# Kernel optimization log

Measured on AMD Instinct MI355X. Metric: run time of the kernel, lower is better.

The kernel has to match this reference:

```python
import jax, jax.numpy as jnp
import numpy as np

N = 50000      # nodes
E = 800000     # edges
G = 512        # graphs in batch
F0 = 92        # orig atom feature len
F = 64         # atom_fea_len
NB = 41        # nbr_fea_len
H = 128        # h_fea_len
NCONV = 3
EPS = 1e-5


def setup_inputs() -> dict:
    key = jax.random.key(0)
    ks = jax.random.split(key, 16)
    s = 0.05
    inp = {
        "x": jax.random.normal(ks[0], (N, F0), jnp.float32),
        "edge_index": jax.random.randint(ks[1], (2, E), 0, N),
        "edge_attr": jax.random.normal(ks[2], (E, NB), jnp.float32),
        "batch": jnp.sort(jax.random.randint(ks[3], (N,), 0, G)),
        # embedding (only applied at the first conv, when x width == F0)
        "emb_W": jax.random.normal(ks[4], (F0, F), jnp.float32) * s,
        "emb_b": jnp.zeros((F,), jnp.float32),
        # per-conv-layer params, stacked on leading axis
        "bn1_g": jnp.ones((NCONV, F), jnp.float32),
        "bn1_b": jnp.zeros((NCONV, F), jnp.float32),
        "bn2_g": jnp.ones((NCONV, F), jnp.float32),
        "bn2_b": jnp.zeros((NCONV, F), jnp.float32),
        "lnf_W": jax.random.normal(ks[5], (NCONV, 2 * F + NB, F), jnp.float32) * s,
        "lnf_b": jnp.zeros((NCONV, F), jnp.float32),
        "lns_W": jax.random.normal(ks[6], (NCONV, 2 * F + NB, F), jnp.float32) * s,
        "lns_b": jnp.zeros((NCONV, F), jnp.float32),
        # readout MLP
        "fc1_W": jax.random.normal(ks[7], (F, H), jnp.float32) * s,
        "fc1_b": jnp.zeros((H,), jnp.float32),
        "out_W": jax.random.normal(ks[8], (H, 1), jnp.float32) * s,
        "out_b": jnp.zeros((1,), jnp.float32),
    }
    return inp


def _batchnorm(x, g, b):
    # training-mode BatchNorm1d: batch stats over node dim, biased variance
    mean = jnp.mean(x, axis=0)
    var = jnp.var(x, axis=0)
    return (x - mean) * jax.lax.rsqrt(var + EPS) * g + b


def _cgconv(x, edge_index, edge_attr, bn1_g, bn1_b, bn2_g, bn2_b, Wf, bf, Ws, bs):
    x = _batchnorm(x, bn1_g, bn1_b)
    # flow='target_to_source': x_i = x[edge_index[0]], x_j = x[edge_index[1]],
    # aggregation scatter-adds messages to edge_index[0]
    src, dst = edge_index[0], edge_index[1]
    z = jnp.concatenate([x[src], x[dst], edge_attr], axis=-1)   # [E, 2F+NB]
    m = jax.nn.sigmoid(z @ Wf + bf) * jax.nn.softplus(z @ Ws + bs)
    agg = jax.ops.segment_sum(m, src, num_segments=x.shape[0])  # [N, F]
    out = _batchnorm(agg, bn2_g, bn2_b) + x
    return jax.nn.softplus(out)


def reference(x, edge_index, edge_attr, batch, emb_W, emb_b,
              bn1_g, bn1_b, bn2_g, bn2_b, lnf_W, lnf_b, lns_W, lns_b,
              fc1_W, fc1_b, out_W, out_b):
    h = x @ emb_W + emb_b  # first conv applies embedding (x width == F0)
    for i in range(NCONV):
        h = _cgconv(h, edge_index, edge_attr,
                    bn1_g[i], bn1_b[i], bn2_g[i], bn2_b[i],
                    lnf_W[i], lnf_b[i], lns_W[i], lns_b[i])
    # global mean pool per graph
    sums = jax.ops.segment_sum(h, batch, num_segments=G)
    cnts = jax.ops.segment_sum(jnp.ones((h.shape[0], 1), h.dtype), batch, num_segments=G)
    crys = sums / jnp.maximum(cnts, 1.0)                         # [G, F]
    crys = jax.nn.softplus(jax.nn.softplus(crys) @ fc1_W + fc1_b)
    return crys @ out_W + out_b                                  # [G, 1]
```

## Files before the change

kernel.cpp:

```cpp
#include <hip/hip_runtime.h>

#define NN 50000
#define NE 800000
#define NG 512
#define F0 92
#define FF 64
#define NB 41
#define HH 128

__device__ __forceinline__ float softplusf(float x) {
    return fmaxf(x, 0.f) + __logf(1.f + __expf(-fabsf(x)));
}
__device__ __forceinline__ float sigmoidf(float x) {
    return __fdividef(1.f, 1.f + __expf(-x));
}

__global__ __launch_bounds__(256) void emb_kernel(
    const float* __restrict__ x, const float* __restrict__ W,
    const float* __restrict__ bias, float* __restrict__ h)
{
    __shared__ float sx[4][F0];
    const int lane = threadIdx.x & 63;
    const int w = threadIdx.x >> 6;
    float wr[F0];
#pragma unroll
    for (int k = 0; k < F0; ++k) wr[k] = W[k * FF + lane];
    const float bv = bias[lane];
    const int nit = NN / 4;
    for (int it = blockIdx.x; it < nit; it += gridDim.x) {
        const int n = it * 4 + w;
        if (lane < 46) {
            sx[w][lane * 2]     = x[n * F0 + lane * 2];
            sx[w][lane * 2 + 1] = x[n * F0 + lane * 2 + 1];
        }
        __syncthreads();
        float acc = bv;
#pragma unroll
        for (int k4 = 0; k4 < F0 / 4; ++k4) {
            float4 q = *(const float4*)&sx[w][k4 * 4];
            acc = fmaf(q.x, wr[k4 * 4 + 0], acc);
            acc = fmaf(q.y, wr[k4 * 4 + 1], acc);
            acc = fmaf(q.z, wr[k4 * 4 + 2], acc);
            acc = fmaf(q.w, wr[k4 * 4 + 3], acc);
        }
        h[n * FF + lane] = acc;
        __syncthreads();
    }
}

__global__ __launch_bounds__(256) void stats_kernel(
    const float* __restrict__ src, float* __restrict__ stats)
{
    __shared__ float sd[2][4][FF];
    const int f = threadIdx.x & 63;
    const int r = threadIdx.x >> 6;
    float s = 0.f, s2 = 0.f;
    for (int n = blockIdx.x * 4 + r; n < NN; n += gridDim.x * 4) {
        float v = src[n * FF + f];
        s += v;
        s2 = fmaf(v, v, s2);
    }
    sd[0][r][f] = s;
    sd[1][r][f] = s2;
    __syncthreads();
    if (threadIdx.x < FF) {
        float ts = sd[0][0][f] + sd[0][1][f] + sd[0][2][f] + sd[0][3][f];
        float t2 = sd[1][0][f] + sd[1][1][f] + sd[1][2][f] + sd[1][3][f];
        atomicAdd(&stats[f], ts);
        atomicAdd(&stats[FF + f], t2);
    }
}

__global__ void finalize_kernel(const float* __restrict__ g, const float* __restrict__ b,
                                float* __restrict__ stats)
{
    const int f = threadIdx.x;
    const float inv = 1.f / (float)NN;
    float mean = stats[f] * inv;
    float var = stats[FF + f] * inv - mean * mean;
    float rstd = rsqrtf(var + 1e-5f);
    float A = rstd * g[f];
    stats[2 * FF + f] = A;
    stats[3 * FF + f] = fmaf(-mean, A, b[f]);
}

__global__ __launch_bounds__(256) void node_kernel(
    const float* __restrict__ h, const float* __restrict__ stats,
    const float* __restrict__ Wf, const float* __restrict__ Ws,
    float* __restrict__ xn,
    float* __restrict__ pSf, float* __restrict__ pDf,
    float* __restrict__ pSs, float* __restrict__ pDs)
{
    __shared__ float sx[4][FF];
    const int lane = threadIdx.x & 63;
    const int w = threadIdx.x >> 6;
    const float* W = (w < 2) ? Wf : Ws;
    const int rowbase = (w & 1) * FF;
    float wr[FF];
#pragma unroll
    for (int k = 0; k < FF; ++k) wr[k] = W[(rowbase + k) * FF + lane];
    const float A = stats[2 * FF + lane];
    const float B = stats[3 * FF + lane];
    float* outp = (w == 0) ? pSf : (w == 1) ? pDf : (w == 2) ? pSs : pDs;
    for (int n = blockIdx.x; n < NN; n += gridDim.x) {
        const float xv = fmaf(h[n * FF + lane], A, B);
        if (w == 0) xn[n * FF + lane] = xv;
        sx[w][lane] = xv;
        __syncthreads();
        float acc = 0.f;
#pragma unroll
        for (int k4 = 0; k4 < FF / 4; ++k4) {
            float4 q = *(const float4*)&sx[w][k4 * 4];
            acc = fmaf(q.x, wr[k4 * 4 + 0], acc);
            acc = fmaf(q.y, wr[k4 * 4 + 1], acc);
            acc = fmaf(q.z, wr[k4 * 4 + 2], acc);
            acc = fmaf(q.w, wr[k4 * 4 + 3], acc);
        }
        outp[n * FF + lane] = acc;
        __syncthreads();
    }
}

__global__ __launch_bounds__(256) void edge_kernel(
    const int* __restrict__ ei, const float* __restrict__ ea,
    const float* __restrict__ Wf, const float* __restrict__ Ws,
    const float* __restrict__ bf, const float* __restrict__ bs,
    const float* __restrict__ pSf, const float* __restrict__ pDf,
    const float* __restrict__ pSs, const float* __restrict__ pDs,
    float* __restrict__ agg)
{
    __shared__ float sea[4][44];
    const int lane = threadIdx.x & 63;
    const int w = threadIdx.x >> 6;
    float wfr[44], wsr[44];
#pragma unroll
    for (int k = 0; k < 44; ++k) {
        wfr[k] = (k < NB) ? Wf[(2 * FF + k) * FF + lane] : 0.f;
        wsr[k] = (k < NB) ? Ws[(2 * FF + k) * FF + lane] : 0.f;
    }
    const float bfv = bf[lane], bsv = bs[lane];
    const int nit = NE / 4;
    for (int it = blockIdx.x; it < nit; it += gridDim.x) {
        const int e = it * 4 + w;
        const int src = ei[e];
        const int dst = ei[NE + e];
        const float gSf = pSf[src * FF + lane];
        const float gDf = pDf[dst * FF + lane];
        const float gSs = pSs[src * FF + lane];
        const float gDs = pDs[dst * FF + lane];
        float v = 0.f;
        if (lane < NB) v = ea[(size_t)e * NB + lane];
        if (lane < 44) sea[w][lane] = v;
        __syncthreads();
        float accF = bfv, accS = bsv;
#pragma unroll
        for (int k4 = 0; k4 < 11; ++k4) {
            float4 q = *(const float4*)&sea[w][k4 * 4];
            accF = fmaf(q.x, wfr[k4 * 4 + 0], accF); accS = fmaf(q.x, wsr[k4 * 4 + 0], accS);
            accF = fmaf(q.y, wfr[k4 * 4 + 1], accF); accS = fmaf(q.y, wsr[k4 * 4 + 1], accS);
            accF = fmaf(q.z, wfr[k4 * 4 + 2], accF); accS = fmaf(q.z, wsr[k4 * 4 + 2], accS);
            accF = fmaf(q.w, wfr[k4 * 4 + 3], accF); accS = fmaf(q.w, wsr[k4 * 4 + 3], accS);
        }
        const float m = sigmoidf(accF + gSf + gDf) * softplusf(accS + gSs + gDs);
        unsafeAtomicAdd(&agg[src * FF + lane], m);
    }
}

__global__ __launch_bounds__(256) void update_kernel(
    const float* __restrict__ agg, const float* __restrict__ xn,
    const float* __restrict__ stats, float* __restrict__ h,
    const int* __restrict__ batch, float* __restrict__ pool,
    float* __restrict__ pcnt, const int do_pool)
{
    const int total = NN * FF;
    for (int idx = blockIdx.x * blockDim.x + threadIdx.x; idx < total;
         idx += gridDim.x * blockDim.x) {
        const int f = idx & 63;
        const int n = idx >> 6;
        const float A = stats[2 * FF + f];
        const float B = stats[3 * FF + f];
        const float v = softplusf(fmaf(agg[idx], A, B) + xn[idx]);
        if (do_pool) {
            const int g = batch[n];
            unsafeAtomicAdd(&pool[g * FF + f], v);
            if (f == 0) unsafeAtomicAdd(&pcnt[g], 1.f);
        } else {
            h[idx] = v;
        }
    }
}

__global__ __launch_bounds__(128) void readout_kernel(
    const float* __restrict__ pool, const float* __restrict__ pcnt,
    const float* __restrict__ fc1W, const float* __restrict__ fc1b,
    const float* __restrict__ outW, const float* __restrict__ outb,
    float* __restrict__ out)
{
    __shared__ float sp[FF];
    __shared__ float red[2];
    const int g = blockIdx.x;
    const int t = threadIdx.x;
    if (t < FF) {
        const float c = fmaxf(pcnt[g], 1.f);
        sp[t] = softplusf(pool[g * FF + t] / c);
    }
    __syncthreads();
    float a = fc1b[t];
#pragma unroll
    for (int k = 0; k < FF; ++k) a = fmaf(sp[k], fc1W[k * HH + t], a);
    float o = softplusf(a) * outW[t];
#pragma unroll
    for (int off = 32; off > 0; off >>= 1) o += __shfl_down(o, off, 64);
    if ((t & 63) == 0) red[t >> 6] = o;
    __syncthreads();
    if (t == 0) out[g] = red[0] + red[1] + outb[0];
}

extern "C" void kernel_launch(void* const* d_in, const int* in_sizes, int n_in,
                              void* d_out, int out_size, void* d_ws, size_t ws_size,
                              hipStream_t stream)
{
    const float* x     = (const float*)d_in[0];
    const int*   ei    = (const int*)  d_in[1];
    const float* ea    = (const float*)d_in[2];
    const int*   batch = (const int*)  d_in[3];
    const float* embW  = (const float*)d_in[4];
    const float* embb  = (const float*)d_in[5];
    const float* bn1g  = (const float*)d_in[6];
    const float* bn1b  = (const float*)d_in[7];
    const float* bn2g  = (const float*)d_in[8];
    const float* bn2b  = (const float*)d_in[9];
    const float* lnfW  = (const float*)d_in[10];
    const float* lnfb  = (const float*)d_in[11];
    const float* lnsW  = (const float*)d_in[12];
    const float* lnsb  = (const float*)d_in[13];
    const float* fc1W  = (const float*)d_in[14];
    const float* fc1b  = (const float*)d_in[15];
    const float* outW  = (const float*)d_in[16];
    const float* outb  = (const float*)d_in[17];

    float* ws    = (float*)d_ws;
    float* h     = ws;
    float* xn    = h    + (size_t)NN * FF;
    float* pSf   = xn   + (size_t)NN * FF;
    float* pDf   = pSf  + (size_t)NN * FF;
    float* pSs   = pDf  + (size_t)NN * FF;
    float* pDs   = pSs  + (size_t)NN * FF;
    float* agg   = pDs  + (size_t)NN * FF;
    float* stats = agg  + (size_t)NN * FF;
    float* pool  = stats + 4 * FF;
    float* pcnt  = pool + (size_t)NG * FF;

    hipMemsetAsync(pool, 0, (NG * FF + NG) * sizeof(float), stream);
    emb_kernel<<<1024, 256, 0, stream>>>(x, embW, embb, h);

    for (int i = 0; i < 3; ++i) {
        const float* Wf  = lnfW + (size_t)i * 169 * FF;
        const float* Wsp = lnsW + (size_t)i * 169 * FF;
        hipMemsetAsync(stats, 0, 2 * FF * sizeof(float), stream);
        stats_kernel<<<256, 256, 0, stream>>>(h, stats);
        finalize_kernel<<<1, 64, 0, stream>>>(bn1g + i * FF, bn1b + i * FF, stats);
        node_kernel<<<1024, 256, 0, stream>>>(h, stats, Wf, Wsp, xn, pSf, pDf, pSs, pDs);
        hipMemsetAsync(agg, 0, (size_t)NN * FF * sizeof(float), stream);
        edge_kernel<<<2048, 256, 0, stream>>>(ei, ea, Wf, Wsp, lnfb + i * FF, lnsb + i * FF,
                                              pSf, pDf, pSs, pDs, agg);
        hipMemsetAsync(stats, 0, 2 * FF * sizeof(float), stream);
        stats_kernel<<<256, 256, 0, stream>>>(agg, stats);
        finalize_kernel<<<1, 64, 0, stream>>>(bn2g + i * FF, bn2b + i * FF, stats);
        update_kernel<<<2048, 256, 0, stream>>>(agg, xn, stats, h, batch, pool, pcnt,
                                                (i == 2) ? 1 : 0);
    }
    readout_kernel<<<NG, HH, 0, stream>>>(pool, pcnt, fc1W, fc1b, outW, outb, (float*)d_out);
}
```

Baseline: 1.145 ms.

## Interleave node projections, drop LDS staging in edge kernel, fold biases

Node projections are now stored interleaved as [N,64,2], with the filter and core halves side by side, so each edge gathers one float2 per endpoint instead of four scalar loads. The edge kernel reads edge attributes straight from global memory with unaligned vector loads instead of staging them in LDS. This removes a __syncthreads per edge iteration and moves the edge index to a scalar register. Biases are folded into the node-side precompute, and launch bounds hint 4 blocks per CU. The risks are unaligned vector loads on 41-float rows and a larger projection buffer footprint.

```diff
diff --git a/kernel.cpp b/kernel.cpp
--- a/kernel.cpp
+++ b/kernel.cpp
@@ -8,6 +8,8 @@
 #define NB 41
 #define HH 128
 
+typedef float f4u __attribute__((ext_vector_type(4), aligned(4)));
+
 __device__ __forceinline__ float softplusf(float x) {
     return fmaxf(x, 0.f) + __logf(1.f + __expf(-fabsf(x)));
 }
@@ -15,7 +17,7 @@
     return __fdividef(1.f, 1.f + __expf(-x));
 }
 
-__global__ __launch_bounds__(256) void emb_kernel(
+__global__ __launch_bounds__(256, 4) void emb_kernel(
     const float* __restrict__ x, const float* __restrict__ W,
     const float* __restrict__ bias, float* __restrict__ h)
 {
@@ -84,12 +86,11 @@
     stats[3 * FF + f] = fmaf(-mean, A, b[f]);
 }
 
-__global__ __launch_bounds__(256) void node_kernel(
+__global__ __launch_bounds__(256, 4) void node_kernel(
     const float* __restrict__ h, const float* __restrict__ stats,
     const float* __restrict__ Wf, const float* __restrict__ Ws,
-    float* __restrict__ xn,
-    float* __restrict__ pSf, float* __restrict__ pDf,
-    float* __restrict__ pSs, float* __restrict__ pDs)
+    const float* __restrict__ bf, const float* __restrict__ bs,
+    float* __restrict__ xn, float* __restrict__ pS, float* __restrict__ pD)
 {
     __shared__ float sx[4][FF];
     const int lane = threadIdx.x & 63;
@@ -101,13 +102,16 @@
     for (int k = 0; k < FF; ++k) wr[k] = W[(rowbase + k) * FF + lane];
     const float A = stats[2 * FF + lane];
     const float B = stats[3 * FF + lane];
-    float* outp = (w == 0) ? pSf : (w == 1) ? pDf : (w == 2) ? pSs : pDs;
+    float bias = 0.f;
+    if (w == 0) bias = bf[lane];
+    if (w == 2) bias = bs[lane];
+    float* outp = ((w & 1) ? pD : pS) + ((w >> 1) & 1);
     for (int n = blockIdx.x; n < NN; n += gridDim.x) {
         const float xv = fmaf(h[n * FF + lane], A, B);
         if (w == 0) xn[n * FF + lane] = xv;
         sx[w][lane] = xv;
         __syncthreads();
-        float acc = 0.f;
+        float acc = bias;
 #pragma unroll
         for (int k4 = 0; k4 < FF / 4; ++k4) {
             float4 q = *(const float4*)&sx[w][k4 * 4];
@@ -116,53 +120,49 @@
             acc = fmaf(q.z, wr[k4 * 4 + 2], acc);
             acc = fmaf(q.w, wr[k4 * 4 + 3], acc);
         }
-        outp[n * FF + lane] = acc;
-        __syncthreads();
-    }
-}
-
-__global__ __launch_bounds__(256) void edge_kernel(
+        outp[(size_t)n * 128 + 2 * lane] = acc;
+        __syncthreads();
+    }
+}
+
+__global__ __launch_bounds__(256, 4) void edge_kernel(
     const int* __restrict__ ei, const float* __restrict__ ea,
     const float* __restrict__ Wf, const float* __restrict__ Ws,
-    const float* __restrict__ bf, const float* __restrict__ bs,
-    const float* __restrict__ pSf, const float* __restrict__ pDf,
-    const float* __restrict__ pSs, const float* __restrict__ pDs,
+    const float* __restrict__ pS, const float* __restrict__ pD,
     float* __restrict__ agg)
 {
-    __shared__ float sea[4][44];
     const int lane = threadIdx.x & 63;
     const int w = threadIdx.x >> 6;
-    float wfr[44], wsr[44];
-#pragma unroll
-    for (int k = 0; k < 44; ++k) {
-        wfr[k] = (k < NB) ? Wf[(2 * FF + k) * FF + lane] : 0.f;
-        wsr[k] = (k < NB) ? Ws[(2 * FF + k) * FF + lane] : 0.f;
-    }
-    const float bfv = bf[lane], bsv = bs[lane];
+    float wfr[NB], wsr[NB];
+#pragma unroll
+    for (int k = 0; k < NB; ++k) {
+        wfr[k] = Wf[(2 * FF + k) * FF + lane];
+        wsr[k] = Ws[(2 * FF + k) * FF + lane];
+    }
     const int nit = NE / 4;
     for (int it = blockIdx.x; it < nit; it += gridDim.x) {
-        const int e = it * 4 + w;
+        const int e = __builtin_amdgcn_readfirstlane(it * 4 + w);
         const int src = ei[e];
         const int dst = ei[NE + e];
-        const float gSf = pSf[src * FF + lane];
-        const float gDf = pDf[dst * FF + lane];
-        const float gSs = pSs[src * FF + lane];
-        const float gDs = pDs[dst * FF + lane];
-        float v = 0.f;
-        if (lane < NB) v = ea[(size_t)e * NB + lane];
-        if (lane < 44) sea[w][lane] = v;
-        __syncthreads();
-        float accF = bfv, accS = bsv;
-#pragma unroll
-        for (int k4 = 0; k4 < 11; ++k4) {
-            float4 q = *(const float4*)&sea[w][k4 * 4];
+        const float2 gS = *(const float2*)(pS + (size_t)src * 128 + 2 * lane);
+        const float2 gD = *(const float2*)(pD + (size_t)dst * 128 + 2 * lane);
+        const float* er = ea + (size_t)e * NB;
+        float accF = 0.f, accS = 0.f;
+#pragma unroll
+        for (int k4 = 0; k4 < 10; ++k4) {
+            const f4u q = *(const f4u*)(er + k4 * 4);
             accF = fmaf(q.x, wfr[k4 * 4 + 0], accF); accS = fmaf(q.x, wsr[k4 * 4 + 0], accS);
             accF = fmaf(q.y, wfr[k4 * 4 + 1], accF); accS = fmaf(q.y, wsr[k4 * 4 + 1], accS);
             accF = fmaf(q.z, wfr[k4 * 4 + 2], accF); accS = fmaf(q.z, wsr[k4 * 4 + 2], accS);
             accF = fmaf(q.w, wfr[k4 * 4 + 3], accF); accS = fmaf(q.w, wsr[k4 * 4 + 3], accS);
         }
-        const float m = sigmoidf(accF + gSf + gDf) * softplusf(accS + gSs + gDs);
-        unsafeAtomicAdd(&agg[src * FF + lane], m);
+        const float q40 = er[40];
+        accF = fmaf(q40, wfr[40], accF);
+        accS = fmaf(q40, wsr[40], accS);
+        accF += gS.x + gD.x;
+        accS += gS.y + gD.y;
+        const float m = sigmoidf(accF) * softplusf(accS);
+        unsafeAtomicAdd(&agg[(size_t)src * FF + lane], m);
     }
 }
 
@@ -242,11 +242,9 @@
     float* ws    = (float*)d_ws;
     float* h     = ws;
     float* xn    = h    + (size_t)NN * FF;
-    float* pSf   = xn   + (size_t)NN * FF;
-    float* pDf   = pSf  + (size_t)NN * FF;
-    float* pSs   = pDf  + (size_t)NN * FF;
-    float* pDs   = pSs  + (size_t)NN * FF;
-    float* agg   = pDs  + (size_t)NN * FF;
+    float* pS    = xn   + (size_t)NN * FF;
+    float* pD    = pS   + (size_t)NN * 128;
+    float* agg   = pD   + (size_t)NN * 128;
     float* stats = agg  + (size_t)NN * FF;
     float* pool  = stats + 4 * FF;
     float* pcnt  = pool + (size_t)NG * FF;
@@ -260,10 +258,10 @@
         hipMemsetAsync(stats, 0, 2 * FF * sizeof(float), stream);
         stats_kernel<<<256, 256, 0, stream>>>(h, stats);
         finalize_kernel<<<1, 64, 0, stream>>>(bn1g + i * FF, bn1b + i * FF, stats);
-        node_kernel<<<1024, 256, 0, stream>>>(h, stats, Wf, Wsp, xn, pSf, pDf, pSs, pDs);
+        node_kernel<<<1024, 256, 0, stream>>>(h, stats, Wf, Wsp,
+                                              lnfb + i * FF, lnsb + i * FF, xn, pS, pD);
         hipMemsetAsync(agg, 0, (size_t)NN * FF * sizeof(float), stream);
-        edge_kernel<<<2048, 256, 0, stream>>>(ei, ea, Wf, Wsp, lnfb + i * FF, lnsb + i * FF,
-                                              pSf, pDf, pSs, pDs, agg);
+        edge_kernel<<<2048, 256, 0, stream>>>(ei, ea, Wf, Wsp, pS, pD, agg);
         hipMemsetAsync(stats, 0, 2 * FF * sizeof(float), stream);
         stats_kernel<<<256, 256, 0, stream>>>(agg, stats);
         finalize_kernel<<<1, 64, 0, stream>>>(bn2g + i * FF, bn2b + i * FF, stats);
```

After: 1.071 ms. 6.5% less time.
